# Kernel optimization log

Hardware: AMD Instinct MI355X
Metric: run time of the kernel (lower is better)

Reference implementation:

```python
import jax, jax.numpy as jnp
import numpy as np

N = 50000       # nodes
E = 1600000     # edges (avg degree 32)
IN_DIM = 128
H_DIM = 128
OUT_DIM = 10
G = 512         # graphs in batch
K = 10          # APPNP propagation steps
ALPHA = 0.1


def _linear_params(key, fan_in, fan_out):
    kw, kb = jax.random.split(key)
    bound = 1.0 / np.sqrt(fan_in)
    W = jax.random.uniform(kw, (fan_in, fan_out), jnp.float32, -bound, bound)
    b = jax.random.uniform(kb, (fan_out,), jnp.float32, -bound, bound)
    return W, b


def setup_inputs() -> dict:
    key = jax.random.key(0)
    ks = jax.random.split(key, 8)
    features = jax.random.normal(ks[0], (IN_DIM, N), jnp.float32)
    edge_index = jax.random.randint(ks[1], (2, E), 0, N, jnp.int32)
    edge_weight = jax.random.uniform(ks[2], (E,), jnp.float32)
    batch = jnp.sort(jax.random.randint(ks[3], (N,), 0, G, jnp.int32))
    W1, b1 = _linear_params(ks[4], IN_DIM, H_DIM)
    W2, b2 = _linear_params(ks[5], H_DIM, H_DIM)
    V0w, V0b = _linear_params(ks[6], H_DIM, H_DIM)
    V1w, V1b = _linear_params(ks[7], H_DIM, OUT_DIM)
    return {"features": features, "edge_weight": edge_weight,
            "W1": W1, "b1": b1, "W2": W2, "b2": b2,
            "V0w": V0w, "V0b": V0b, "V1w": V1w, "V1b": V1b,
            "edge_index": edge_index, "batch": batch}


def reference(features, edge_weight, W1, b1, W2, b2, V0w, V0b, V1w, V1b,
              edge_index, batch):
    # features: [in_dim, N] -> nodes-first, matching `x = features.T`
    x = features.T @ W1 + b1          # [N, H]
    x = x @ W2 + b2                   # [N, H]

    src, dst = edge_index[0], edge_index[1]
    h = x  # teleport term
    # APPNP, normalize=False, dropout=0: x <- (1-a)*A_w x + a*h, K times
    for _ in range(K):
        msgs = edge_weight[:, None] * x[src]                  # [E, H]
        agg = jax.ops.segment_sum(msgs, dst, num_segments=N)  # [N, H]
        x = (1.0 - ALPHA) * agg + ALPHA * h

    pooled = jax.ops.segment_sum(x, batch, num_segments=G)    # [G, H]
    y = jax.nn.relu(pooled @ V0w + V0b)
    # dropout inactive in eval mode
    y = y @ V1w + V1b                                         # [G, OUT]
    return jax.nn.log_softmax(y, axis=1)
```

## Files before the change

### kernel.cpp

```cpp
#include <hip/hip_runtime.h>
#include <hip/hip_fp16.h>
#include <cstdint>

#define HD    128
#define OUTD  10
#define NG    512
#define KSTEPS 10

typedef unsigned short ushort_t;
typedef unsigned int   uint_t;
typedef unsigned char  uchar_t;
typedef float vf2 __attribute__((ext_vector_type(2)));

__device__ __forceinline__ float bf_lo(uint_t u) { return __uint_as_float(u << 16); }
__device__ __forceinline__ float bf_hi(uint_t u) { return __uint_as_float(u & 0xFFFF0000u); }
__device__ __forceinline__ uint_t f2bf_rne(float f) {
    uint_t u = __float_as_uint(f);
    return (u + 0x7FFFu + ((u >> 16) & 1u)) >> 16;
}
__device__ __forceinline__ uint_t pack_bf2(float lo, float hi) {
    return f2bf_rne(lo) | (f2bf_rne(hi) << 16);
}

__device__ __forceinline__ vf2 pk_fma(vf2 a, vf2 b, vf2 c) {
    vf2 d;
    asm("v_pk_fma_f32 %0, %1, %2, %3" : "=v"(d) : "v"(a), "v"(b), "v"(c));
    return d;
}

__global__ void wc_kernel(const float* __restrict__ W1, const float* __restrict__ b1,
                          const float* __restrict__ W2, const float* __restrict__ b2,
                          float* __restrict__ Wc, float* __restrict__ bc) {
    int idx = blockIdx.x * 256 + threadIdx.x;
    int d = idx >> 7, j = idx & 127;
    float s = 0.f;
    for (int t = 0; t < HD; t++) s += W1[d * HD + t] * W2[t * HD + j];
    Wc[idx] = s;
    if (idx < HD) {
        float sb = b2[idx];
        for (int t = 0; t < HD; t++) sb += b1[t] * W2[t * HD + idx];
        bc[idx] = sb;
    }
}

#define FNT 64
#define FDC 32
__global__ void __launch_bounds__(256) feat_kernel(
        const float* __restrict__ feat, const float* __restrict__ Wc,
        const float* __restrict__ bc, ushort_t* __restrict__ h, int N) {
    __shared__ float fch[FDC * FNT];
    __shared__ float wch[FDC * HD];
    int t = threadIdx.x;
    int nb0 = blockIdx.x * FNT;
    int tj = t & 15, tn = t >> 4;
    int j0 = tj * 8, n0 = tn * 4;

    float acc[4][8];
    #pragma unroll
    for (int a = 0; a < 4; a++)
        #pragma unroll
        for (int b = 0; b < 8; b++) acc[a][b] = 0.f;

    for (int dc = 0; dc < HD; dc += FDC) {
        #pragma unroll
        for (int k = 0; k < (FDC * FNT) / 256; k++) {
            int l = k * 256 + t;
            int dd = l >> 6, n = l & 63;
            int nn = nb0 + n;
            fch[l] = (nn < N) ? feat[(size_t)(dc + dd) * N + nn] : 0.f;
        }
        #pragma unroll
        for (int k = 0; k < (FDC * HD) / 256; k++) {
            int l = k * 256 + t;
            int dd = l >> 7, j = l & 127;
            wch[l] = Wc[(dc + dd) * HD + j];
        }
        __syncthreads();
        for (int dd = 0; dd < FDC; dd++) {
            const float* fr = &fch[dd * FNT + n0];
            const float* wr = &wch[dd * HD + j0];
            float fv[4], wv[8];
            #pragma unroll
            for (int a = 0; a < 4; a++) fv[a] = fr[a];
            #pragma unroll
            for (int b = 0; b < 8; b++) wv[b] = wr[b];
            #pragma unroll
            for (int a = 0; a < 4; a++)
                #pragma unroll
                for (int b = 0; b < 8; b++) acc[a][b] += fv[a] * wv[b];
        }
        __syncthreads();
    }

    float bv[8];
    #pragma unroll
    for (int b = 0; b < 8; b++) bv[b] = bc[j0 + b];
    #pragma unroll
    for (int a = 0; a < 4; a++) {
        int n = nb0 + n0 + a;
        if (n < N) {
            uint4 ov;
            ov.x = pack_bf2(acc[a][0] + bv[0], acc[a][1] + bv[1]);
            ov.y = pack_bf2(acc[a][2] + bv[2], acc[a][3] + bv[3]);
            ov.z = pack_bf2(acc[a][4] + bv[4], acc[a][5] + bv[5]);
            ov.w = pack_bf2(acc[a][6] + bv[6], acc[a][7] + bv[7]);
            *(uint4*)(h + (size_t)n * HD + j0) = ov;
        }
    }
}


__global__ void __launch_bounds__(256) bcount_kernel(
        const int* __restrict__ ei, int* __restrict__ gbhist, int E, int chunk) {
    __shared__ int lh[256];
    int b = blockIdx.x, t = threadIdx.x;
    lh[t] = 0;
    __syncthreads();
    int lo = b * chunk, hi = min(E, lo + chunk);
    for (int i = lo + t; i < hi; i += 256) atomicAdd(&lh[ei[E + i] >> 8], 1);
    __syncthreads();
    if (lh[t]) atomicAdd(&gbhist[t], lh[t]);
}

__global__ void bscan_kernel(const int* __restrict__ gbhist, int* __restrict__ bucket_base,
                             int* __restrict__ bcursor, int NBK, int E) {
    __shared__ int sm[256];
    int t = threadIdx.x;
    int v = (t < NBK) ? gbhist[t] : 0;
    sm[t] = v;
    __syncthreads();
    for (int off = 1; off < 256; off <<= 1) {
        int u = (t >= off) ? sm[t - off] : 0;
        __syncthreads();
        sm[t] += u;
        __syncthreads();
    }
    int excl = sm[t] - v;
    if (t < NBK) { bucket_base[t] = excl; bcursor[t] = excl; }
    if (t == 0) bucket_base[NBK] = E;
}

__global__ void __launch_bounds__(256) bscatter_kernel(
        const int* __restrict__ ei, const float* __restrict__ ewt,
        int* __restrict__ bcursor, uint_t* __restrict__ rec_tmp,
        uchar_t* __restrict__ dlo_tmp, int E, int chunk) {
    __shared__ int lh[256];
    __shared__ int lcur[256];
    int b = blockIdx.x, t = threadIdx.x;
    lh[t] = 0;
    __syncthreads();
    int lo = b * chunk, hi = min(E, lo + chunk);
    for (int i = lo + t; i < hi; i += 256) atomicAdd(&lh[ei[E + i] >> 8], 1);
    __syncthreads();
    lcur[t] = lh[t] ? atomicAdd(&bcursor[t], lh[t]) : 0;
    __syncthreads();
    for (int i = lo + t; i < hi; i += 256) {
        int d = ei[E + i];
        int p = atomicAdd(&lcur[d >> 8], 1);
        rec_tmp[p] = ((uint_t)ei[i] << 16) |
                     (uint_t)__half_as_ushort(__float2half(ewt[i]));
        dlo_tmp[p] = (uchar_t)(d & 255);
    }
}

__global__ void __launch_bounds__(256) bsort_kernel(
        const uint_t* __restrict__ rec_tmp, const uchar_t* __restrict__ dlo_tmp,
        const int* __restrict__ bucket_base, int* __restrict__ row_ptr,
        uint_t* __restrict__ erec, int N, int E) {
    __shared__ int hist[256];
    __shared__ int scn[256];
    __shared__ int cur[256];
    int b = blockIdx.x, t = threadIdx.x;
    int lo = bucket_base[b], hi = bucket_base[b + 1];
    hist[t] = 0;
    __syncthreads();
    for (int i = lo + t; i < hi; i += 256) atomicAdd(&hist[dlo_tmp[i]], 1);
    __syncthreads();
    int v = hist[t];
    scn[t] = v;
    __syncthreads();
    for (int off = 1; off < 256; off <<= 1) {
        int u = (t >= off) ? scn[t - off] : 0;
        __syncthreads();
        scn[t] += u;
        __syncthreads();
    }
    int excl = lo + scn[t] - v;
    int node = (b << 8) + t;
    if (node < N) row_ptr[node] = excl;
    if (b == 0 && t == 0) row_ptr[N] = E;
    cur[t] = excl;
    __syncthreads();
    for (int i = lo + t; i < hi; i += 256) {
        int p = atomicAdd(&cur[dlo_tmp[i]], 1);
        erec[p] = rec_tmp[i];
    }
}

__global__ void __launch_bounds__(256) prop_kernel(
        const ushort_t* __restrict__ xs, ushort_t* __restrict__ xd,
        const ushort_t* __restrict__ h, const int* __restrict__ row_ptr,
        const uint_t* __restrict__ erec, int N) {
    int wid = threadIdx.x >> 6, lane = threadIdx.x & 63;
    int node = blockIdx.x * 4 + wid;
    if (node >= N) return;
    int rs = row_ptr[node], re = row_ptr[node + 1];
    int grp = lane >> 4;
    int sub = lane & 15;

    vf2 acc2[4];
    #pragma unroll
    for (int i = 0; i < 4; i++) acc2[i] = (vf2)0.f;

    uint_t p[8];
    #pragma unroll
    for (int u = 0; u < 8; u++) {
        int e = rs + grp + 4 * u;
        p[u] = (e < re) ? erec[e] : 0u;
    }

    for (int base = rs; base < re; base += 32) {
        uint_t q[8];
        #pragma unroll
        for (int u = 0; u < 8; u++) {
            int e = base + 32 + grp + 4 * u;
            q[u] = (e < re) ? erec[e] : 0u;
        }
        #pragma unroll
        for (int u = 0; u < 8; u++) {
            int   s = (int)(p[u] >> 16);
            float w = __half2float(__ushort_as_half((ushort_t)(p[u] & 0xFFFFu)));
            vf2 w2; w2.x = w; w2.y = w;
            uint4 a = ((const uint4*)(xs + (size_t)s * HD))[sub];
            vf2 x0; x0.x = bf_lo(a.x); x0.y = bf_hi(a.x);
            vf2 x1; x1.x = bf_lo(a.y); x1.y = bf_hi(a.y);
            vf2 x2; x2.x = bf_lo(a.z); x2.y = bf_hi(a.z);
            vf2 x3; x3.x = bf_lo(a.w); x3.y = bf_hi(a.w);
            acc2[0] = pk_fma(w2, x0, acc2[0]);
            acc2[1] = pk_fma(w2, x1, acc2[1]);
            acc2[2] = pk_fma(w2, x2, acc2[2]);
            acc2[3] = pk_fma(w2, x3, acc2[3]);
        }
        #pragma unroll
        for (int u = 0; u < 8; u++) p[u] = q[u];
    }

    float acc[8];
    #pragma unroll
    for (int i = 0; i < 4; i++) { acc[2 * i] = acc2[i].x; acc[2 * i + 1] = acc2[i].y; }

    #pragma unroll
    for (int off = 32; off >= 16; off >>= 1) {
        #pragma unroll
        for (int i = 0; i < 8; i++) acc[i] += __shfl_down(acc[i], off);
    }

    if (grp == 0) {
        uint4 hv = ((const uint4*)(h + (size_t)node * HD))[sub];
        float hf[8];
        hf[0] = bf_lo(hv.x); hf[1] = bf_hi(hv.x);
        hf[2] = bf_lo(hv.y); hf[3] = bf_hi(hv.y);
        hf[4] = bf_lo(hv.z); hf[5] = bf_hi(hv.z);
        hf[6] = bf_lo(hv.w); hf[7] = bf_hi(hv.w);
        float o[8];
        #pragma unroll
        for (int i = 0; i < 8; i++) o[i] = 0.9f * acc[i] + 0.1f * hf[i];
        uint4 ov;
        ov.x = pack_bf2(o[0], o[1]);
        ov.y = pack_bf2(o[2], o[3]);
        ov.z = pack_bf2(o[4], o[5]);
        ov.w = pack_bf2(o[6], o[7]);
        ((uint4*)(xd + (size_t)node * HD))[sub] = ov;
    }
}

#define POOL_CHUNK 128
__global__ void pool_kernel(const ushort_t* __restrict__ x, const int* __restrict__ batch,
                            float* __restrict__ pooled, int N) {
    int j = threadIdx.x;
    int n0 = blockIdx.x * POOL_CHUNK;
    if (n0 >= N) return;
    int n1 = min(n0 + POOL_CHUNK, N);
    int cur = batch[n0];
    float acc = 0.f;
    for (int n = n0; n < n1; n++) {
        int g = batch[n];
        if (g != cur) {
            atomicAdd(&pooled[cur * HD + j], acc);
            acc = 0.f; cur = g;
        }
        acc += __uint_as_float(((uint_t)x[(size_t)n * HD + j]) << 16);
    }
    atomicAdd(&pooled[cur * HD + j], acc);
}

__global__ void head_kernel(const float* __restrict__ pooled, const float* __restrict__ V0w,
                            const float* __restrict__ V0b, const float* __restrict__ V1w,
                            const float* __restrict__ V1b, float* __restrict__ out) {
    __shared__ float prow[HD];
    __shared__ float y1[HD];
    __shared__ float y2[OUTD];
    __shared__ float lse;
    int g = blockIdx.x, j = threadIdx.x;
    prow[j] = pooled[g * HD + j];
    __syncthreads();
    float a = V0b[j];
    for (int d = 0; d < HD; d++) a += prow[d] * V0w[d * HD + j];
    y1[j] = a > 0.f ? a : 0.f;
    __syncthreads();
    if (j < OUTD) {
        float a2 = V1b[j];
        for (int t = 0; t < HD; t++) a2 += y1[t] * V1w[t * OUTD + j];
        y2[j] = a2;
    }
    __syncthreads();
    if (j == 0) {
        float m = y2[0];
        for (int o = 1; o < OUTD; o++) m = fmaxf(m, y2[o]);
        float s = 0.f;
        for (int o = 0; o < OUTD; o++) s += expf(y2[o] - m);
        lse = m + logf(s);
    }
    __syncthreads();
    if (j < OUTD) out[g * OUTD + j] = y2[j] - lse;
}

extern "C" void kernel_launch(void* const* d_in, const int* in_sizes, int n_in,
                              void* d_out, int out_size, void* d_ws, size_t ws_size,
                              hipStream_t stream) {
    const float* feat = (const float*)d_in[0];
    const float* ewt  = (const float*)d_in[1];
    const float* W1   = (const float*)d_in[2];
    const float* b1   = (const float*)d_in[3];
    const float* W2   = (const float*)d_in[4];
    const float* b2   = (const float*)d_in[5];
    const float* V0w  = (const float*)d_in[6];
    const float* V0b  = (const float*)d_in[7];
    const float* V1w  = (const float*)d_in[8];
    const float* V1b  = (const float*)d_in[9];
    const int*   ei   = (const int*)d_in[10];
    const int*   batch= (const int*)d_in[11];
    const int E = in_sizes[1];
    const int N = in_sizes[11];
    float* out = (float*)d_out;

    char* ws = (char*)d_ws;
    size_t off = 0;
    auto alloc = [&](size_t bytes) -> char* {
        char* p = ws + off;
        off = (off + bytes + 255) & ~(size_t)255;
        return p;
    };
    float*    Wc        = (float*)alloc((size_t)HD * HD * 4);
    float*    bc        = (float*)alloc((size_t)HD * 4);
    ushort_t* hb        = (ushort_t*)alloc((size_t)N * HD * 2);
    ushort_t* xA        = (ushort_t*)alloc((size_t)N * HD * 2);
    ushort_t* xB        = (ushort_t*)alloc((size_t)N * HD * 2);
    float*    pooled    = (float*)alloc((size_t)NG * HD * 4);
    int*      row_ptr   = (int*)alloc((size_t)(N + 1) * 4);
    int*      gbhist    = (int*)alloc((size_t)256 * 4);
    int*      bucket_b  = (int*)alloc((size_t)257 * 4);
    int*      bcursor   = (int*)alloc((size_t)256 * 4);
    uint_t*   rec_tmp   = (uint_t*)alloc((size_t)E * 4);
    uchar_t*  dlo_tmp   = (uchar_t*)alloc((size_t)E);
    uint_t*   erec      = (uint_t*)alloc((size_t)E * 4);
    (void)ws_size;

    hipMemsetAsync(gbhist, 0, (size_t)256 * 4, stream);
    hipMemsetAsync(pooled, 0, (size_t)NG * HD * 4, stream);

    const int NBK    = (N + 255) >> 8;
    const int SBLK   = 256;
    const int chunk  = (E + SBLK - 1) / SBLK;

    wc_kernel<<<64, 256, 0, stream>>>(W1, b1, W2, b2, Wc, bc);
    feat_kernel<<<(N + FNT - 1) / FNT, 256, 0, stream>>>(feat, Wc, bc, hb, N);
    bcount_kernel<<<SBLK, 256, 0, stream>>>(ei, gbhist, E, chunk);
    bscan_kernel<<<1, 256, 0, stream>>>(gbhist, bucket_b, bcursor, NBK, E);
    bscatter_kernel<<<SBLK, 256, 0, stream>>>(ei, ewt, bcursor, rec_tmp, dlo_tmp, E, chunk);
    bsort_kernel<<<NBK, 256, 0, stream>>>(rec_tmp, dlo_tmp, bucket_b, row_ptr, erec, N, E);

    const ushort_t* src = hb;
    ushort_t* dst = xA;
    for (int k = 0; k < KSTEPS; k++) {
        prop_kernel<<<(N + 3) / 4, 256, 0, stream>>>(src, dst, hb, row_ptr, erec, N);
        src = dst;
        dst = (dst == xA) ? xB : xA;
    }

    pool_kernel<<<(N + POOL_CHUNK - 1) / POOL_CHUNK, HD, 0, stream>>>(src, batch, pooled, N);
    head_kernel<<<NG, HD, 0, stream>>>(pooled, V0w, V0b, V1w, V1b, out);
}
```

Measured before the change: 743.9 us.

## Process two nodes per wavefront with interleaved software-pipelined gathers

Each wavefront now aggregates two destination nodes, alternating between them so that the neighbour-row gathers for one node are in flight while FMAs run for the other. The aim is more memory-level parallelism per wave to hide gather latency in the propagation kernel. Edge weights are now stored as bf16 instead of fp16, which makes decoding a single shift. The trade-offs are higher register pressure, and the loop runs to the larger of the two degrees, so some lanes sit idle when the two nodes have different degrees.

```diff
diff --git a/kernel.cpp b/kernel.cpp
--- a/kernel.cpp
+++ b/kernel.cpp
@@ -157,8 +157,7 @@
     for (int i = lo + t; i < hi; i += 256) {
         int d = ei[E + i];
         int p = atomicAdd(&lcur[d >> 8], 1);
-        rec_tmp[p] = ((uint_t)ei[i] << 16) |
-                     (uint_t)__half_as_ushort(__float2half(ewt[i]));
+        rec_tmp[p] = ((uint_t)ei[i] << 16) | f2bf_rne(ewt[i]);
         dlo_tmp[p] = (uchar_t)(d & 255);
     }
 }
@@ -202,75 +201,134 @@
         const ushort_t* __restrict__ h, const int* __restrict__ row_ptr,
         const uint_t* __restrict__ erec, int N) {
     int wid = threadIdx.x >> 6, lane = threadIdx.x & 63;
-    int node = blockIdx.x * 4 + wid;
-    if (node >= N) return;
-    int rs = row_ptr[node], re = row_ptr[node + 1];
+    int pair = blockIdx.x * 4 + wid;
+    int nA = pair * 2;
+    if (nA >= N) return;
+    int nB = nA + 1;
+    bool hasB = (nB < N);
+    int rsA = row_ptr[nA], reA = row_ptr[nA + 1];
+    int rsB = hasB ? row_ptr[nB] : 0;
+    int reB = hasB ? row_ptr[nB + 1] : 0;
     int grp = lane >> 4;
     int sub = lane & 15;
 
-    vf2 acc2[4];
-    #pragma unroll
-    for (int i = 0; i < 4; i++) acc2[i] = (vf2)0.f;
-
-    uint_t p[8];
+    vf2 accA[4], accB[4];
+    #pragma unroll
+    for (int i = 0; i < 4; i++) { accA[i] = (vf2)0.f; accB[i] = (vf2)0.f; }
+
+    uint_t rA[8], rB[8];
+    uint4  xA_[8], xB_[8];
+
     #pragma unroll
     for (int u = 0; u < 8; u++) {
-        int e = rs + grp + 4 * u;
-        p[u] = (e < re) ? erec[e] : 0u;
-    }
-
-    for (int base = rs; base < re; base += 32) {
-        uint_t q[8];
+        int eA = rsA + grp + 4 * u;
+        int eB = rsB + grp + 4 * u;
+        rA[u] = (eA < reA) ? erec[eA] : 0u;
+        rB[u] = (eB < reB) ? erec[eB] : 0u;
+    }
+    #pragma unroll
+    for (int u = 0; u < 8; u++)
+        xA_[u] = ((const uint4*)(xs + (size_t)(rA[u] >> 16) * HD))[sub];
+
+    int span = max(reA - rsA, reB - rsB);
+    int bA = rsA, bB = rsB;
+    for (int done = 0; done < span; done += 32) {
+        float wA[8], wB[8];
+        int sB[8];
         #pragma unroll
         for (int u = 0; u < 8; u++) {
-            int e = base + 32 + grp + 4 * u;
-            q[u] = (e < re) ? erec[e] : 0u;
-        }
+            wA[u] = __uint_as_float(rA[u] << 16);
+            wB[u] = __uint_as_float(rB[u] << 16);
+            sB[u] = (int)(rB[u] >> 16);
+        }
+        #pragma unroll
+        for (int u = 0; u < 8; u++)
+            xB_[u] = ((const uint4*)(xs + (size_t)sB[u] * HD))[sub];
         #pragma unroll
         for (int u = 0; u < 8; u++) {
-            int   s = (int)(p[u] >> 16);
-            float w = __half2float(__ushort_as_half((ushort_t)(p[u] & 0xFFFFu)));
-            vf2 w2; w2.x = w; w2.y = w;
-            uint4 a = ((const uint4*)(xs + (size_t)s * HD))[sub];
+            int eA = bA + 32 + grp + 4 * u;
+            int eB = bB + 32 + grp + 4 * u;
+            rA[u] = (eA < reA) ? erec[eA] : 0u;
+            rB[u] = (eB < reB) ? erec[eB] : 0u;
+        }
+        #pragma unroll
+        for (int u = 0; u < 8; u++) {
+            vf2 w2; w2.x = wA[u]; w2.y = wA[u];
+            uint4 a = xA_[u];
             vf2 x0; x0.x = bf_lo(a.x); x0.y = bf_hi(a.x);
             vf2 x1; x1.x = bf_lo(a.y); x1.y = bf_hi(a.y);
             vf2 x2; x2.x = bf_lo(a.z); x2.y = bf_hi(a.z);
             vf2 x3; x3.x = bf_lo(a.w); x3.y = bf_hi(a.w);
-            acc2[0] = pk_fma(w2, x0, acc2[0]);
-            acc2[1] = pk_fma(w2, x1, acc2[1]);
-            acc2[2] = pk_fma(w2, x2, acc2[2]);
-            acc2[3] = pk_fma(w2, x3, acc2[3]);
-        }
-        #pragma unroll
-        for (int u = 0; u < 8; u++) p[u] = q[u];
-    }
-
-    float acc[8];
-    #pragma unroll
-    for (int i = 0; i < 4; i++) { acc[2 * i] = acc2[i].x; acc[2 * i + 1] = acc2[i].y; }
-
+            accA[0] = pk_fma(w2, x0, accA[0]);
+            accA[1] = pk_fma(w2, x1, accA[1]);
+            accA[2] = pk_fma(w2, x2, accA[2]);
+            accA[3] = pk_fma(w2, x3, accA[3]);
+        }
+        #pragma unroll
+        for (int u = 0; u < 8; u++)
+            xA_[u] = ((const uint4*)(xs + (size_t)(rA[u] >> 16) * HD))[sub];
+        #pragma unroll
+        for (int u = 0; u < 8; u++) {
+            vf2 w2; w2.x = wB[u]; w2.y = wB[u];
+            uint4 a = xB_[u];
+            vf2 x0; x0.x = bf_lo(a.x); x0.y = bf_hi(a.x);
+            vf2 x1; x1.x = bf_lo(a.y); x1.y = bf_hi(a.y);
+            vf2 x2; x2.x = bf_lo(a.z); x2.y = bf_hi(a.z);
+            vf2 x3; x3.x = bf_lo(a.w); x3.y = bf_hi(a.w);
+            accB[0] = pk_fma(w2, x0, accB[0]);
+            accB[1] = pk_fma(w2, x1, accB[1]);
+            accB[2] = pk_fma(w2, x2, accB[2]);
+            accB[3] = pk_fma(w2, x3, accB[3]);
+        }
+        bA += 32; bB += 32;
+    }
+
+    float aA[8], aB[8];
+    #pragma unroll
+    for (int i = 0; i < 4; i++) {
+        aA[2 * i] = accA[i].x; aA[2 * i + 1] = accA[i].y;
+        aB[2 * i] = accB[i].x; aB[2 * i + 1] = accB[i].y;
+    }
     #pragma unroll
     for (int off = 32; off >= 16; off >>= 1) {
         #pragma unroll
-        for (int i = 0; i < 8; i++) acc[i] += __shfl_down(acc[i], off);
+        for (int i = 0; i < 8; i++) {
+            aA[i] += __shfl_down(aA[i], off);
+            aB[i] += __shfl_down(aB[i], off);
+        }
     }
 
     if (grp == 0) {
-        uint4 hv = ((const uint4*)(h + (size_t)node * HD))[sub];
-        float hf[8];
-        hf[0] = bf_lo(hv.x); hf[1] = bf_hi(hv.x);
-        hf[2] = bf_lo(hv.y); hf[3] = bf_hi(hv.y);
-        hf[4] = bf_lo(hv.z); hf[5] = bf_hi(hv.z);
-        hf[6] = bf_lo(hv.w); hf[7] = bf_hi(hv.w);
+        uint4 hvA = ((const uint4*)(h + (size_t)nA * HD))[sub];
         float o[8];
-        #pragma unroll
-        for (int i = 0; i < 8; i++) o[i] = 0.9f * acc[i] + 0.1f * hf[i];
+        o[0] = 0.9f * aA[0] + 0.1f * bf_lo(hvA.x);
+        o[1] = 0.9f * aA[1] + 0.1f * bf_hi(hvA.x);
+        o[2] = 0.9f * aA[2] + 0.1f * bf_lo(hvA.y);
+        o[3] = 0.9f * aA[3] + 0.1f * bf_hi(hvA.y);
+        o[4] = 0.9f * aA[4] + 0.1f * bf_lo(hvA.z);
+        o[5] = 0.9f * aA[5] + 0.1f * bf_hi(hvA.z);
+        o[6] = 0.9f * aA[6] + 0.1f * bf_lo(hvA.w);
+        o[7] = 0.9f * aA[7] + 0.1f * bf_hi(hvA.w);
         uint4 ov;
-        ov.x = pack_bf2(o[0], o[1]);
-        ov.y = pack_bf2(o[2], o[3]);
-        ov.z = pack_bf2(o[4], o[5]);
-        ov.w = pack_bf2(o[6], o[7]);
-        ((uint4*)(xd + (size_t)node * HD))[sub] = ov;
+        ov.x = pack_bf2(o[0], o[1]); ov.y = pack_bf2(o[2], o[3]);
+        ov.z = pack_bf2(o[4], o[5]); ov.w = pack_bf2(o[6], o[7]);
+        ((uint4*)(xd + (size_t)nA * HD))[sub] = ov;
+        if (hasB) {
+            uint4 hvB = ((const uint4*)(h + (size_t)nB * HD))[sub];
+            float p[8];
+            p[0] = 0.9f * aB[0] + 0.1f * bf_lo(hvB.x);
+            p[1] = 0.9f * aB[1] + 0.1f * bf_hi(hvB.x);
+            p[2] = 0.9f * aB[2] + 0.1f * bf_lo(hvB.y);
+            p[3] = 0.9f * aB[3] + 0.1f * bf_hi(hvB.y);
+            p[4] = 0.9f * aB[4] + 0.1f * bf_lo(hvB.z);
+            p[5] = 0.9f * aB[5] + 0.1f * bf_hi(hvB.z);
+            p[6] = 0.9f * aB[6] + 0.1f * bf_lo(hvB.w);
+            p[7] = 0.9f * aB[7] + 0.1f * bf_hi(hvB.w);
+            uint4 pv;
+            pv.x = pack_bf2(p[0], p[1]); pv.y = pack_bf2(p[2], p[3]);
+            pv.z = pack_bf2(p[4], p[5]); pv.w = pack_bf2(p[6], p[7]);
+            ((uint4*)(xd + (size_t)nB * HD))[sub] = pv;
+        }
     }
 }
 
@@ -383,7 +441,7 @@
     const ushort_t* src = hb;
     ushort_t* dst = xA;
     for (int k = 0; k < KSTEPS; k++) {
-        prop_kernel<<<(N + 3) / 4, 256, 0, stream>>>(src, dst, hb, row_ptr, erec, N);
+        prop_kernel<<<(N + 7) / 8, 256, 0, stream>>>(src, dst, hb, row_ptr, erec, N);
         src = dst;
         dst = (dst == xA) ? xB : xA;
     }
```

New measurement: 809.9 us. 8.9% more time.

## Software-pipeline row gathers in propagation and store edge weights as bf16

Applied to the files above, without the earlier changes.

Restructures the propagation loop into a double-buffered A/B pipeline. Edge records are prefetched two stages ahead and the gathered source rows one stage ahead, so row loads overlap the FMAs of the previous chunk. Each stage now handles 16 edges instead of 32. The teleport row is loaded before the loop, and edge weights are stored as bf16 so decoding is a single shift. The cost is higher register pressure from the buffered uint4 rows and coarser weight precision (bf16 instead of fp16).

```diff
diff --git a/kernel.cpp b/kernel.cpp
--- a/kernel.cpp
+++ b/kernel.cpp
@@ -157,8 +157,7 @@
     for (int i = lo + t; i < hi; i += 256) {
         int d = ei[E + i];
         int p = atomicAdd(&lcur[d >> 8], 1);
-        rec_tmp[p] = ((uint_t)ei[i] << 16) |
-                     (uint_t)__half_as_ushort(__float2half(ewt[i]));
+        rec_tmp[p] = ((uint_t)ei[i] << 16) | f2bf_rne(ewt[i]);
         dlo_tmp[p] = (uchar_t)(d & 255);
     }
 }
@@ -197,6 +196,7 @@
     }
 }
 
+#define PU 4
 __global__ void __launch_bounds__(256) prop_kernel(
         const ushort_t* __restrict__ xs, ushort_t* __restrict__ xd,
         const ushort_t* __restrict__ h, const int* __restrict__ row_ptr,
@@ -208,30 +208,47 @@
     int grp = lane >> 4;
     int sub = lane & 15;
 
+    uint4 hv = make_uint4(0u, 0u, 0u, 0u);
+    if (grp == 0) hv = ((const uint4*)(h + (size_t)node * HD))[sub];
+
     vf2 acc2[4];
     #pragma unroll
     for (int i = 0; i < 4; i++) acc2[i] = (vf2)0.f;
 
-    uint_t p[8];
-    #pragma unroll
-    for (int u = 0; u < 8; u++) {
+    uint_t recA[PU], recB[PU];
+    uint4  rowA[PU], rowB[PU];
+
+    #pragma unroll
+    for (int u = 0; u < PU; u++) {
         int e = rs + grp + 4 * u;
-        p[u] = (e < re) ? erec[e] : 0u;
-    }
-
-    for (int base = rs; base < re; base += 32) {
-        uint_t q[8];
-        #pragma unroll
-        for (int u = 0; u < 8; u++) {
+        recA[u] = (e < re) ? erec[e] : 0u;
+    }
+    #pragma unroll
+    for (int u = 0; u < PU; u++)
+        rowA[u] = ((const uint4*)(xs + (size_t)(recA[u] >> 16) * HD))[sub];
+    #pragma unroll
+    for (int u = 0; u < PU; u++) {
+        int e = rs + 16 + grp + 4 * u;
+        recB[u] = (e < re) ? erec[e] : 0u;
+    }
+
+    int base = rs;
+    for (;;) {
+        #pragma unroll
+        for (int u = 0; u < PU; u++)
+            rowB[u] = ((const uint4*)(xs + (size_t)(recB[u] >> 16) * HD))[sub];
+        float wA[PU];
+        #pragma unroll
+        for (int u = 0; u < PU; u++) wA[u] = __uint_as_float(recA[u] << 16);
+        #pragma unroll
+        for (int u = 0; u < PU; u++) {
             int e = base + 32 + grp + 4 * u;
-            q[u] = (e < re) ? erec[e] : 0u;
-        }
-        #pragma unroll
-        for (int u = 0; u < 8; u++) {
-            int   s = (int)(p[u] >> 16);
-            float w = __half2float(__ushort_as_half((ushort_t)(p[u] & 0xFFFFu)));
-            vf2 w2; w2.x = w; w2.y = w;
-            uint4 a = ((const uint4*)(xs + (size_t)s * HD))[sub];
+            recA[u] = (e < re) ? erec[e] : 0u;
+        }
+        #pragma unroll
+        for (int u = 0; u < PU; u++) {
+            vf2 w2; w2.x = wA[u]; w2.y = wA[u];
+            uint4 a = rowA[u];
             vf2 x0; x0.x = bf_lo(a.x); x0.y = bf_hi(a.x);
             vf2 x1; x1.x = bf_lo(a.y); x1.y = bf_hi(a.y);
             vf2 x2; x2.x = bf_lo(a.z); x2.y = bf_hi(a.z);
@@ -241,8 +258,34 @@
             acc2[2] = pk_fma(w2, x2, acc2[2]);
             acc2[3] = pk_fma(w2, x3, acc2[3]);
         }
-        #pragma unroll
-        for (int u = 0; u < 8; u++) p[u] = q[u];
+        base += 16;
+        if (base >= re) break;
+        #pragma unroll
+        for (int u = 0; u < PU; u++)
+            rowA[u] = ((const uint4*)(xs + (size_t)(recA[u] >> 16) * HD))[sub];
+        float wB[PU];
+        #pragma unroll
+        for (int u = 0; u < PU; u++) wB[u] = __uint_as_float(recB[u] << 16);
+        #pragma unroll
+        for (int u = 0; u < PU; u++) {
+            int e = base + 32 + grp + 4 * u;
+            recB[u] = (e < re) ? erec[e] : 0u;
+        }
+        #pragma unroll
+        for (int u = 0; u < PU; u++) {
+            vf2 w2; w2.x = wB[u]; w2.y = wB[u];
+            uint4 a = rowB[u];
+            vf2 x0; x0.x = bf_lo(a.x); x0.y = bf_hi(a.x);
+            vf2 x1; x1.x = bf_lo(a.y); x1.y = bf_hi(a.y);
+            vf2 x2; x2.x = bf_lo(a.z); x2.y = bf_hi(a.z);
+            vf2 x3; x3.x = bf_lo(a.w); x3.y = bf_hi(a.w);
+            acc2[0] = pk_fma(w2, x0, acc2[0]);
+            acc2[1] = pk_fma(w2, x1, acc2[1]);
+            acc2[2] = pk_fma(w2, x2, acc2[2]);
+            acc2[3] = pk_fma(w2, x3, acc2[3]);
+        }
+        base += 16;
+        if (base >= re) break;
     }
 
     float acc[8];
@@ -256,15 +299,15 @@
     }
 
     if (grp == 0) {
-        uint4 hv = ((const uint4*)(h + (size_t)node * HD))[sub];
-        float hf[8];
-        hf[0] = bf_lo(hv.x); hf[1] = bf_hi(hv.x);
-        hf[2] = bf_lo(hv.y); hf[3] = bf_hi(hv.y);
-        hf[4] = bf_lo(hv.z); hf[5] = bf_hi(hv.z);
-        hf[6] = bf_lo(hv.w); hf[7] = bf_hi(hv.w);
         float o[8];
-        #pragma unroll
-        for (int i = 0; i < 8; i++) o[i] = 0.9f * acc[i] + 0.1f * hf[i];
+        o[0] = 0.9f * acc[0] + 0.1f * bf_lo(hv.x);
+        o[1] = 0.9f * acc[1] + 0.1f * bf_hi(hv.x);
+        o[2] = 0.9f * acc[2] + 0.1f * bf_lo(hv.y);
+        o[3] = 0.9f * acc[3] + 0.1f * bf_hi(hv.y);
+        o[4] = 0.9f * acc[4] + 0.1f * bf_lo(hv.z);
+        o[5] = 0.9f * acc[5] + 0.1f * bf_hi(hv.z);
+        o[6] = 0.9f * acc[6] + 0.1f * bf_lo(hv.w);
+        o[7] = 0.9f * acc[7] + 0.1f * bf_hi(hv.w);
         uint4 ov;
         ov.x = pack_bf2(o[0], o[1]);
         ov.y = pack_bf2(o[2], o[3]);
```

Measured after the change: 740.8 us. No clear change (-0.4%).

## Split propagation into two feature-half passes and store edge weights as bf16

Applied to the files above, without the earlier changes.

Each APPNP step now runs as two kernel launches, each gathering and writing only 64 of the 128 feature columns. The smaller per-pass gather working set (half of the node feature table) is meant to fit better in L2/MALL and raise cache hit rates on the random source-row gathers. The cost is that the edge records and row pointers are read twice per step and the launch count doubles. Edge weights are also stored as bf16 instead of fp16, so they decode with a single shift, at the price of lower weight precision.

```diff
diff --git a/kernel.cpp b/kernel.cpp
--- a/kernel.cpp
+++ b/kernel.cpp
@@ -157,8 +157,7 @@
     for (int i = lo + t; i < hi; i += 256) {
         int d = ei[E + i];
         int p = atomicAdd(&lcur[d >> 8], 1);
-        rec_tmp[p] = ((uint_t)ei[i] << 16) |
-                     (uint_t)__half_as_ushort(__float2half(ewt[i]));
+        rec_tmp[p] = ((uint_t)ei[i] << 16) | f2bf_rne(ewt[i]);
         dlo_tmp[p] = (uchar_t)(d & 255);
     }
 }
@@ -200,7 +199,7 @@
 __global__ void __launch_bounds__(256) prop_kernel(
         const ushort_t* __restrict__ xs, ushort_t* __restrict__ xd,
         const ushort_t* __restrict__ h, const int* __restrict__ row_ptr,
-        const uint_t* __restrict__ erec, int N) {
+        const uint_t* __restrict__ erec, int N, int dofs) {
     int wid = threadIdx.x >> 6, lane = threadIdx.x & 63;
     int node = blockIdx.x * 4 + wid;
     if (node >= N) return;
@@ -208,9 +207,13 @@
     int grp = lane >> 4;
     int sub = lane & 15;
 
-    vf2 acc2[4];
-    #pragma unroll
-    for (int i = 0; i < 4; i++) acc2[i] = (vf2)0.f;
+    const ushort_t* xsl = xs + dofs;
+
+    uint2 hv = make_uint2(0u, 0u);
+    if (grp == 0) hv = ((const uint2*)(h + dofs + (size_t)node * HD))[sub];
+
+    vf2 acc2[2];
+    acc2[0] = (vf2)0.f; acc2[1] = (vf2)0.f;
 
     uint_t p[8];
     #pragma unroll
@@ -229,48 +232,38 @@
         #pragma unroll
         for (int u = 0; u < 8; u++) {
             int   s = (int)(p[u] >> 16);
-            float w = __half2float(__ushort_as_half((ushort_t)(p[u] & 0xFFFFu)));
+            float w = __uint_as_float(p[u] << 16);
             vf2 w2; w2.x = w; w2.y = w;
-            uint4 a = ((const uint4*)(xs + (size_t)s * HD))[sub];
+            uint2 a = ((const uint2*)(xsl + (size_t)s * HD))[sub];
             vf2 x0; x0.x = bf_lo(a.x); x0.y = bf_hi(a.x);
             vf2 x1; x1.x = bf_lo(a.y); x1.y = bf_hi(a.y);
-            vf2 x2; x2.x = bf_lo(a.z); x2.y = bf_hi(a.z);
-            vf2 x3; x3.x = bf_lo(a.w); x3.y = bf_hi(a.w);
             acc2[0] = pk_fma(w2, x0, acc2[0]);
             acc2[1] = pk_fma(w2, x1, acc2[1]);
-            acc2[2] = pk_fma(w2, x2, acc2[2]);
-            acc2[3] = pk_fma(w2, x3, acc2[3]);
         }
         #pragma unroll
         for (int u = 0; u < 8; u++) p[u] = q[u];
     }
 
-    float acc[8];
-    #pragma unroll
-    for (int i = 0; i < 4; i++) { acc[2 * i] = acc2[i].x; acc[2 * i + 1] = acc2[i].y; }
+    float acc[4];
+    acc[0] = acc2[0].x; acc[1] = acc2[0].y;
+    acc[2] = acc2[1].x; acc[3] = acc2[1].y;
 
     #pragma unroll
     for (int off = 32; off >= 16; off >>= 1) {
         #pragma unroll
-        for (int i = 0; i < 8; i++) acc[i] += __shfl_down(acc[i], off);
+        for (int i = 0; i < 4; i++) acc[i] += __shfl_down(acc[i], off);
     }
 
     if (grp == 0) {
-        uint4 hv = ((const uint4*)(h + (size_t)node * HD))[sub];
-        float hf[8];
-        hf[0] = bf_lo(hv.x); hf[1] = bf_hi(hv.x);
-        hf[2] = bf_lo(hv.y); hf[3] = bf_hi(hv.y);
-        hf[4] = bf_lo(hv.z); hf[5] = bf_hi(hv.z);
-        hf[6] = bf_lo(hv.w); hf[7] = bf_hi(hv.w);
-        float o[8];
-        #pragma unroll
-        for (int i = 0; i < 8; i++) o[i] = 0.9f * acc[i] + 0.1f * hf[i];
-        uint4 ov;
+        float o[4];
+        o[0] = 0.9f * acc[0] + 0.1f * bf_lo(hv.x);
+        o[1] = 0.9f * acc[1] + 0.1f * bf_hi(hv.x);
+        o[2] = 0.9f * acc[2] + 0.1f * bf_lo(hv.y);
+        o[3] = 0.9f * acc[3] + 0.1f * bf_hi(hv.y);
+        uint2 ov;
         ov.x = pack_bf2(o[0], o[1]);
         ov.y = pack_bf2(o[2], o[3]);
-        ov.z = pack_bf2(o[4], o[5]);
-        ov.w = pack_bf2(o[6], o[7]);
-        ((uint4*)(xd + (size_t)node * HD))[sub] = ov;
+        ((uint2*)(xd + dofs + (size_t)node * HD))[sub] = ov;
     }
 }
 
@@ -383,7 +376,8 @@
     const ushort_t* src = hb;
     ushort_t* dst = xA;
     for (int k = 0; k < KSTEPS; k++) {
-        prop_kernel<<<(N + 3) / 4, 256, 0, stream>>>(src, dst, hb, row_ptr, erec, N);
+        prop_kernel<<<(N + 3) / 4, 256, 0, stream>>>(src, dst, hb, row_ptr, erec, N, 0);
+        prop_kernel<<<(N + 3) / 4, 256, 0, stream>>>(src, dst, hb, row_ptr, erec, N, 64);
         src = dst;
         dst = (dst == xA) ? xB : xA;
     }
```

After: 808.6 us. +8.7%, slower.
